# Kernel tuning notes

Measured on AMD Instinct MI355X. Metric: run time of the kernel, lower is better.

## Reference

```python
import jax, jax.numpy as jnp
import numpy as np

C = 512
CQ = C // 8
B, H, W = 8, 64, 64


def conv1x1(x, w, b):
    # x: [B,Cin,H,W], w: [Cout,Cin], b: [Cout]
    return jnp.einsum('bchw,oc->bohw', x, w) + b[None, :, None, None]


def setup_inputs() -> dict:
    key = jax.random.key(0)
    ks = jax.random.split(key, 16)
    s = 0.02
    return {
        'x': jax.random.normal(ks[0], (B, C, H, W), dtype=jnp.float32),
        # position attention params
        'pq_w': jax.random.normal(ks[1], (CQ, C), dtype=jnp.float32) * s,
        'pq_b': jnp.zeros((CQ,), dtype=jnp.float32),
        'pk_w': jax.random.normal(ks[2], (CQ, C), dtype=jnp.float32) * s,
        'pk_b': jnp.zeros((CQ,), dtype=jnp.float32),
        'pv_w': jax.random.normal(ks[3], (C, C), dtype=jnp.float32) * s,
        'pv_b': jnp.zeros((C,), dtype=jnp.float32),
        # channel attention params
        'cq_w': jax.random.normal(ks[4], (CQ, C), dtype=jnp.float32) * s,
        'cq_b': jnp.zeros((CQ,), dtype=jnp.float32),
        'ck_w': jax.random.normal(ks[5], (CQ, C), dtype=jnp.float32) * s,
        'ck_b': jnp.zeros((CQ,), dtype=jnp.float32),
        'cv_w': jax.random.normal(ks[6], (CQ, C), dtype=jnp.float32) * s,
        'cv_b': jnp.zeros((CQ,), dtype=jnp.float32),
        'co_w': jax.random.normal(ks[7], (C, CQ), dtype=jnp.float32) * s,
        'co_b': jnp.zeros((C,), dtype=jnp.float32),
    }


def reference(x, pq_w, pq_b, pk_w, pk_b, pv_w, pv_b,
              cq_w, cq_b, ck_w, ck_b, cv_w, cv_b, co_w, co_b):
    b, c, h, w = x.shape
    hw = h * w

    # ---- Position attention ----
    q = conv1x1(x, pq_w, pq_b).reshape(b, CQ, hw)   # [B,Cq,HW]
    k = conv1x1(x, pk_w, pk_b).reshape(b, CQ, hw)   # [B,Cq,HW]
    v = conv1x1(x, pv_w, pv_b).reshape(b, c, hw)    # [B,C,HW]
    # energy[b,i,j] = sum_c q[b,c,i] * k[b,c,j]; softmax over j
    energy = jnp.einsum('bci,bcj->bij', q, k)       # [B,HW,HW]
    attn = jax.nn.softmax(energy, axis=-1)
    # out[b,c,j] = sum_i v[b,c,i] * attn[b,i,j]  (value @ attention)
    pos_out = jnp.einsum('bci,bij->bcj', v, attn).reshape(b, c, h, w)

    # ---- Channel attention ----
    cq = conv1x1(x, cq_w, cq_b).reshape(b, CQ, hw)  # [B,Cq,HW]
    ck = conv1x1(x, ck_w, ck_b).reshape(b, CQ, hw)  # [B,Cq,HW]
    cv = conv1x1(x, cv_w, cv_b).reshape(b, CQ, hw)  # [B,Cq,HW]
    c_energy = jnp.einsum('bpn,bqn->bpq', cq, ck)   # [B,Cq,Cq]
    c_attn = jax.nn.softmax(c_energy, axis=-1)
    c_out = jnp.einsum('bpq,bqn->bpn', c_attn, cv).reshape(b, CQ, h, w)
    chan_out = conv1x1(c_out, co_w, co_b)           # [B,C,H,W]

    return pos_out + chan_out
```

## Files before the change

### kernel.cpp

```cpp
#include <hip/hip_runtime.h>
#include <stdint.h>


#define LOG2E 1.44269504088896340736f

typedef __attribute__((ext_vector_type(8))) __bf16 bf16x8;
typedef __attribute__((ext_vector_type(4))) float floatx4;
typedef __attribute__((ext_vector_type(2))) float floatx2;
typedef __attribute__((ext_vector_type(2))) unsigned int uint2v;

static __device__ __forceinline__ unsigned short f2bf(float f) {
    union { float f; uint32_t u; } v; v.f = f;
    uint32_t r = v.u + 0x7fffu + ((v.u >> 16) & 1u);
    return (unsigned short)(r >> 16);
}

static __device__ __forceinline__ unsigned int pack_bf16(float a, float b) {
    union { float f; uint32_t u; } x, y; x.f = a; y.f = b;
    return __builtin_amdgcn_perm(y.u + 0x8000u, x.u + 0x8000u, 0x07060302u);
}

template<int BM, int BN, bool OUT_BF16, bool ATOMIC, int SPECIAL = 0>
__global__ __launch_bounds__(256) void tn_gemm(
    const unsigned short* __restrict__ A, int lda, long sA,
    const unsigned short* __restrict__ B, int ldb, long sB,
    void* __restrict__ C, int ldc, long sC,
    const float* __restrict__ bias_m, const float* __restrict__ bias_n,
    const float* __restrict__ scale_n, long sScale,
    int K, int kchunks)
{
    constexpr int PK = 72;
    __shared__ unsigned short As[BM * PK];
    __shared__ unsigned short Bs[BN * PK];
    const int bz = blockIdx.z;
    const int b  = bz / kchunks;
    const int kc = bz % kchunks;
    const int m0 = blockIdx.y * BM;
    const int n0 = blockIdx.x * BN;
    const unsigned short* Ab = A + (long)b * sA + (long)m0 * lda + (long)kc * K;
    const unsigned short* Bb = B + (long)b * sB + (long)n0 * ldb + (long)kc * K;
    const int tid = threadIdx.x;
    const int lane = tid & 63, wave = tid >> 6;
    const int l15 = lane & 15, quad = lane >> 4;
    constexpr int NT  = BN / 16;
    constexpr int MPW = BM / 64;
    constexpr int AL  = BM / 32;
    constexpr int BL  = BN / 32;

    const floatx4 vz = {0.f, 0.f, 0.f, 0.f};
    floatx4 acc[MPW][NT];
    for (int i = 0; i < MPW; ++i) for (int j = 0; j < NT; ++j) acc[i][j] = vz;

    const int nK = K >> 6;
    for (int k0 = 0; k0 < nK; ++k0) {
        floatx4 ar[AL], br[BL];
#pragma unroll
        for (int L = 0; L < AL; ++L) {
            int flat = L * 2048 + tid * 8;
            ar[L] = *(const floatx4*)(Ab + (long)(flat >> 6) * lda + (k0 << 6) + (flat & 63));
        }
#pragma unroll
        for (int L = 0; L < BL; ++L) {
            int flat = L * 2048 + tid * 8;
            br[L] = *(const floatx4*)(Bb + (long)(flat >> 6) * ldb + (k0 << 6) + (flat & 63));
        }
        __syncthreads();
#pragma unroll
        for (int L = 0; L < AL; ++L) {
            int flat = L * 2048 + tid * 8;
            *(floatx4*)&As[(flat >> 6) * PK + (flat & 63)] = ar[L];
        }
#pragma unroll
        for (int L = 0; L < BL; ++L) {
            int flat = L * 2048 + tid * 8;
            *(floatx4*)&Bs[(flat >> 6) * PK + (flat & 63)] = br[L];
        }
        __syncthreads();
#pragma unroll
        for (int ks = 0; ks < 2; ++ks) {
            bf16x8 af[MPW];
#pragma unroll
            for (int mi = 0; mi < MPW; ++mi)
                af[mi] = *(const bf16x8*)&As[((wave * MPW + mi) * 16 + l15) * PK + ks * 32 + quad * 8];
#pragma unroll
            for (int nt = 0; nt < NT; ++nt) {
                bf16x8 bf = *(const bf16x8*)&Bs[(nt * 16 + l15) * PK + ks * 32 + quad * 8];
#pragma unroll
                for (int mi = 0; mi < MPW; ++mi)
                    acc[mi][nt] = __builtin_amdgcn_mfma_f32_16x16x32_bf16(af[mi], bf, acc[mi][nt], 0, 0, 0);
            }
        }
    }
#pragma unroll
    for (int mi = 0; mi < MPW; ++mi) {
        const int mb = m0 + (wave * MPW + mi) * 16 + quad * 4;
#pragma unroll
        for (int nt = 0; nt < NT; ++nt) {
            const int n = n0 + nt * 16 + l15;
            const float bn = bias_n ? bias_n[n] : 0.f;
            const float cs = scale_n ? scale_n[(long)b * sScale + n] : 1.f;
            floatx4 a = acc[mi][nt];
#pragma unroll
            for (int r = 0; r < 4; ++r) {
                const int m = mb + r;
                float v = (a[r] + (bias_m ? bias_m[m] : 0.f) + bn) * cs;
                long idx;
                if (SPECIAL == 1)
                    idx = (long)b * sC + ((long)(n >> 7) * 65536 + (m >> 4) * 2048
                        + ((n >> 5) & 3) * 512 + (m & 15) * 32 + ((n >> 3) & 3) * 8 + (n & 7));
                else if (SPECIAL == 2) {
                    if (n < 64)
                        idx = (long)b * sC + ((long)(m >> 4) * 1024 + (n >> 5) * 512
                            + (m & 15) * 32 + ((n >> 3) & 3) * 8 + (n & 7));
                    else
                        idx = (long)b * sC + (long)(n >> 6) * 262144 + (long)m * 64 + (n & 63);
                } else
                    idx = (long)b * sC + (long)m * ldc + n;
                if (ATOMIC)         atomicAdd((float*)C + idx, v);
                else if (OUT_BF16)  ((unsigned short*)C)[idx] = f2bf(v);
                else                ((float*)C)[idx] = v;
            }
        }
    }
}

__global__ __launch_bounds__(512, 4) void rowsum_kernel(
    const unsigned short* __restrict__ qkvT, float* __restrict__ rcl)
{
    __shared__ unsigned short Ks[2][128 * 72];
    const int b  = blockIdx.x;
    const int i0 = blockIdx.y * 128;
    const unsigned short* qv = qkvT + (long)b * 786432;
    const unsigned short* kb = qkvT + (long)b * 786432 + 262144;
    const int tid = threadIdx.x, lane = tid & 63, wave = tid >> 6;
    const int l15 = lane & 15, quad = lane >> 4;

    bf16x8 af[2];
#pragma unroll
    for (int ks = 0; ks < 2; ++ks)
        af[ks] = *(const bf16x8*)(qv + (long)((i0 >> 4) + wave) * 1024 + ks * 512 + (l15 * 4 + quad) * 8);

#pragma unroll
    for (int p = 0; p < 2; ++p) {
        int flat = p * 4096 + tid * 8;
        *(floatx4*)&Ks[0][(flat >> 6) * 72 + (flat & 63)] = *(const floatx4*)(kb + flat);
    }
    float rs[4] = {0.f, 0.f, 0.f, 0.f};
    const floatx4 vz = {0.f, 0.f, 0.f, 0.f};
    __syncthreads();

    for (int jb = 0; jb < 32; ++jb) {
        const int cur = jb & 1;
        floatx4 stage[2];
        if (jb < 31) {
#pragma unroll
            for (int p = 0; p < 2; ++p) {
                int flat = p * 4096 + tid * 8;
                stage[p] = *(const floatx4*)(kb + (jb + 1) * 8192 + flat);
            }
        }
        floatx4 e[8];
#pragma unroll
        for (int nt = 0; nt < 8; ++nt) e[nt] = vz;
#pragma unroll
        for (int ks = 0; ks < 2; ++ks)
#pragma unroll
            for (int nt = 0; nt < 8; ++nt) {
                bf16x8 bf = *(const bf16x8*)&Ks[cur][(nt * 16 + l15) * 72 + ks * 32 + quad * 8];
                e[nt] = __builtin_amdgcn_mfma_f32_16x16x32_bf16(af[ks], bf, e[nt], 0, 0, 0);
            }
#pragma unroll
        for (int nt = 0; nt < 8; ++nt)
#pragma unroll
            for (int r = 0; r < 4; ++r)
                rs[r] += exp2f(e[nt][r]);
        if (jb < 31) {
#pragma unroll
            for (int p = 0; p < 2; ++p) {
                int flat = p * 4096 + tid * 8;
                *(floatx4*)&Ks[1 - cur][(flat >> 6) * 72 + (flat & 63)] = stage[p];
            }
        }
        __syncthreads();
    }
#pragma unroll
    for (int r = 0; r < 4; ++r) {
        float v = rs[r];
        v += __shfl_xor(v, 1); v += __shfl_xor(v, 2);
        v += __shfl_xor(v, 4); v += __shfl_xor(v, 8);
        if (l15 == 0)
            rcl[(long)b * 4096 + i0 + wave * 16 + quad * 4 + r] = 1.0f / v;
    }
}

__global__ __launch_bounds__(512, 4) void pos_attn_kernel(
    const unsigned short* __restrict__ qkvT, const unsigned short* __restrict__ vP,
    const unsigned short* __restrict__ wco, const unsigned short* __restrict__ coT,
    const float* __restrict__ co_b, float* __restrict__ out)
{
    __shared__ unsigned short Ks[64 * 72];
    __shared__ unsigned short Ps[2][64 * 136];
    const int b  = blockIdx.x;
    const int j0 = blockIdx.y * 64;
    const unsigned short* qb = qkvT + (long)b * 786432;
    const unsigned short* kb = qkvT + (long)b * 786432 + 262144 + (long)j0 * 64;
    const unsigned short* vb = vP + (long)b * 512 * 4096;
    const int tid = threadIdx.x, lane = tid & 63, wave = tid >> 6;
    const int l15 = lane & 15, quad = lane >> 4;
    const int il = wave * 16 + quad * 4;
    const int lfrag = (l15 * 4 + quad) * 8;
    const int vfrag = l15 * 32 + quad * 8;

    {
        int flat = tid * 8;
        *(floatx4*)&Ks[(flat >> 6) * 72 + (flat & 63)] = *(const floatx4*)(kb + flat);
    }
    const floatx4 vz = {0.f, 0.f, 0.f, 0.f};
    floatx4 oacc[4][4];
#pragma unroll
    for (int mi = 0; mi < 4; ++mi) for (int nt = 0; nt < 4; ++nt) oacc[mi][nt] = vz;
    __syncthreads();

    auto e_phase = [&](int ib, int buf) {
        const unsigned short* qr = qb + (long)(ib * 8 + wave) * 1024;
        bf16x8 a0 = *(const bf16x8*)(qr + lfrag);
        bf16x8 a1 = *(const bf16x8*)(qr + 512 + lfrag);
        floatx4 e[4];
#pragma unroll
        for (int nt = 0; nt < 4; ++nt) e[nt] = vz;
#pragma unroll
        for (int nt = 0; nt < 4; ++nt) {
            bf16x8 bf = *(const bf16x8*)&Ks[(nt * 16 + l15) * 72 + quad * 8];
            e[nt] = __builtin_amdgcn_mfma_f32_16x16x32_bf16(a0, bf, e[nt], 0, 0, 0);
        }
#pragma unroll
        for (int nt = 0; nt < 4; ++nt) {
            bf16x8 bf = *(const bf16x8*)&Ks[(nt * 16 + l15) * 72 + 32 + quad * 8];
            e[nt] = __builtin_amdgcn_mfma_f32_16x16x32_bf16(a1, bf, e[nt], 0, 0, 0);
        }
#pragma unroll
        for (int nt = 0; nt < 4; ++nt) {
            uint2v p;
            p.x = pack_bf16(exp2f(e[nt][0]), exp2f(e[nt][1]));
            p.y = pack_bf16(exp2f(e[nt][2]), exp2f(e[nt][3]));
            *(uint2v*)&Ps[buf][(nt * 16 + l15) * 136 + il] = p;
        }
    };

    e_phase(0, 0);
    __syncthreads();

    for (int ib = 0; ib < 32; ++ib) {
        const int cur = ib & 1;
        const unsigned short* vt = vb + (long)ib * 65536 + (wave * 4) * 2048 + vfrag;
#pragma unroll
        for (int ks = 0; ks < 4; ++ks) {
            bf16x8 af[4];
#pragma unroll
            for (int mi = 0; mi < 4; ++mi)
                af[mi] = *(const bf16x8*)(vt + mi * 2048 + ks * 512);
#pragma unroll
            for (int nt = 0; nt < 4; ++nt) {
                bf16x8 bf = *(const bf16x8*)&Ps[cur][(nt * 16 + l15) * 136 + ks * 32 + quad * 8];
#pragma unroll
                for (int mi = 0; mi < 4; ++mi)
                    oacc[mi][nt] = __builtin_amdgcn_mfma_f32_16x16x32_bf16(af[mi], bf, oacc[mi][nt], 0, 0, 0);
            }
        }
        if (ib < 31) e_phase(ib + 1, 1 - cur);
        __syncthreads();
    }

    const unsigned short* cob = coT + ((long)b * 4096 + j0) * 64;
#pragma unroll
    for (int ks = 0; ks < 2; ++ks) {
        bf16x8 aw[4];
#pragma unroll
        for (int mi = 0; mi < 4; ++mi)
            aw[mi] = *(const bf16x8*)(wco + (long)((wave * 4 + mi) * 16 + l15) * 64 + ks * 32 + quad * 8);
#pragma unroll
        for (int nt = 0; nt < 4; ++nt) {
            bf16x8 bf = *(const bf16x8*)(cob + (long)(nt * 16 + l15) * 64 + ks * 32 + quad * 8);
#pragma unroll
            for (int mi = 0; mi < 4; ++mi)
                oacc[mi][nt] = __builtin_amdgcn_mfma_f32_16x16x32_bf16(aw[mi], bf, oacc[mi][nt], 0, 0, 0);
        }
    }
#pragma unroll
    for (int mi = 0; mi < 4; ++mi) {
        const int c = (wave * 4 + mi) * 16 + quad * 4;
#pragma unroll
        for (int nt = 0; nt < 4; ++nt) {
            const int j = j0 + nt * 16 + l15;
#pragma unroll
            for (int r = 0; r < 4; ++r)
                out[((long)b * 512 + c + r) * 4096 + j] = oacc[mi][nt][r] + co_b[c + r];
        }
    }
}

__global__ __launch_bounds__(256) void transpose_x(
    const float* __restrict__ x, unsigned short* __restrict__ xT)
{
    __shared__ unsigned short T[64 * 66];
    const int b  = blockIdx.z;
    const int n0 = blockIdx.x * 64;
    const int c0 = blockIdx.y * 64;
    const int tid = threadIdx.x;
    const int r8 = tid >> 5;
    const int col2 = (tid & 31) * 2;
#pragma unroll
    for (int k = 0; k < 8; ++k) {
        const int c = r8 + k * 8;
        floatx2 v = *(const floatx2*)(x + ((long)(b * 512 + c0 + c)) * 4096 + n0 + col2);
        *(unsigned int*)&T[c * 66 + col2] = pack_bf16(v.x, v.y);
    }
    __syncthreads();
#pragma unroll
    for (int k = 0; k < 8; ++k) {
        const int n = r8 + k * 8;
        unsigned int pk = (unsigned int)T[col2 * 66 + n] | ((unsigned int)T[(col2 + 1) * 66 + n] << 16);
        *(unsigned int*)(xT + ((long)(b * 4096 + n0 + n)) * 512 + c0 + col2) = pk;
    }
}

__global__ __launch_bounds__(256) void convert_weights(
    const float* __restrict__ pq_w, const float* __restrict__ pk_w,
    const float* __restrict__ pv_w, const float* __restrict__ cq_w,
    const float* __restrict__ ck_w, const float* __restrict__ cv_w,
    const float* __restrict__ co_w,
    const float* __restrict__ pq_b, const float* __restrict__ pk_b,
    const float* __restrict__ cv_b, const float* __restrict__ cq_b,
    const float* __restrict__ ck_b,
    unsigned short* __restrict__ dst, float* __restrict__ biases)
{
    const int total = 458752;
    const int gtid = blockIdx.x * 256 + threadIdx.x;
    for (int i = gtid; i < total; i += gridDim.x * 256) {
        float v;
        if (i < 98304) {
            int r = i >> 9, k = i & 511;
            if (r < 64)       v = pq_w[r * 512 + k] * LOG2E;
            else if (r < 128) v = pk_w[(r - 64) * 512 + k];
            else              v = cv_w[(r - 128) * 512 + k];
        } else if (i < 163840) {
            int j = i - 98304; int r = j >> 9, k = j & 511;
            v = (r < 64) ? cq_w[r * 512 + k] : ck_w[(r - 64) * 512 + k];
        } else if (i < 425984) v = pv_w[i - 163840];
        else                   v = co_w[i - 425984];
        dst[i] = f2bf(v);
    }
    if (gtid < 320) {
        float v;
        if (gtid < 64)       v = pq_b[gtid] * LOG2E;
        else if (gtid < 128) v = pk_b[gtid - 64];
        else if (gtid < 192) v = cv_b[gtid - 128];
        else if (gtid < 256) v = cq_b[gtid - 192];
        else                 v = ck_b[gtid - 256];
        biases[gtid] = v;
    }
}

__global__ __launch_bounds__(64) void chan_softmax(
    const float* __restrict__ ce, unsigned short* __restrict__ ca)
{
    const int p = blockIdx.x, b = blockIdx.y, q = threadIdx.x;
    const long base = ((long)b * 64 + p) * 64;
    float v = ce[base + q];
    float m = v;
#pragma unroll
    for (int s = 32; s >= 1; s >>= 1) m = fmaxf(m, __shfl_xor(m, s));
    float e = exp2f((v - m) * LOG2E);
    float sum = e;
#pragma unroll
    for (int s = 32; s >= 1; s >>= 1) sum += __shfl_xor(sum, s);
    ca[base + q] = f2bf(e / sum);
}

extern "C" void kernel_launch(void* const* d_in, const int* in_sizes, int n_in,
                              void* d_out, int out_size, void* d_ws, size_t ws_size,
                              hipStream_t stream) {
    const float* x    = (const float*)d_in[0];
    const float* pv_b = (const float*)d_in[6];
    const float* co_b = (const float*)d_in[14];
    float* out = (float*)d_out;
    char* ws = (char*)d_ws;

    constexpr long OFF_XT   = 0;
    constexpr long OFF_QKV  = 33554432;
    constexpr long OFF_VP   = OFF_QKV + 12582912;
    constexpr long OFF_CQCK = OFF_VP + 33554432;
    constexpr long OFF_COT  = OFF_CQCK + 8388608;
    constexpr long OFF_RCL  = OFF_COT + 4194304;
    constexpr long OFF_CE   = OFF_RCL + 131072;
    constexpr long OFF_CAT  = OFF_CE + 131072;
    constexpr long OFF_WB   = OFF_CAT + 65536;
    constexpr long OFF_BIAS = OFF_WB + 917504;

    unsigned short* xT   = (unsigned short*)(ws + OFF_XT);
    unsigned short* qkvT = (unsigned short*)(ws + OFF_QKV);
    unsigned short* vP   = (unsigned short*)(ws + OFF_VP);
    unsigned short* cqck = (unsigned short*)(ws + OFF_CQCK);
    unsigned short* coT  = (unsigned short*)(ws + OFF_COT);
    float*          rcl  = (float*)(ws + OFF_RCL);
    float*          ce   = (float*)(ws + OFF_CE);
    unsigned short* cat  = (unsigned short*)(ws + OFF_CAT);
    unsigned short* wb   = (unsigned short*)(ws + OFF_WB);
    float*          bias = (float*)(ws + OFF_BIAS);
    unsigned short* wqkv  = wb;
    unsigned short* wcqck = wb + 98304;
    unsigned short* wv    = wb + 163840;
    unsigned short* wco   = wb + 425984;
    float* bqkv  = bias;
    float* bcqck = bias + 192;

    convert_weights<<<dim3(64), 256, 0, stream>>>(
        (const float*)d_in[1], (const float*)d_in[3], (const float*)d_in[5],
        (const float*)d_in[7], (const float*)d_in[9], (const float*)d_in[11],
        (const float*)d_in[13],
        (const float*)d_in[2], (const float*)d_in[4], (const float*)d_in[12],
        (const float*)d_in[8], (const float*)d_in[10], wb, bias);
    transpose_x<<<dim3(64, 8, 8), 256, 0, stream>>>(x, xT);

    tn_gemm<128, 192, true, false, 2><<<dim3(1, 32, 8), 256, 0, stream>>>(
        xT, 512, 2097152L, wqkv, 512, 0L, qkvT, 192, 786432L,
        nullptr, bqkv, nullptr, 0L, 512, 1);
    tn_gemm<128, 128, true, false><<<dim3(32, 1, 8), 256, 0, stream>>>(
        wcqck, 512, 0L, xT, 512, 2097152L, cqck, 4096, 524288L,
        bcqck, nullptr, nullptr, 0L, 512, 1);

    rowsum_kernel<<<dim3(8, 32), 512, 0, stream>>>(qkvT, rcl);

    tn_gemm<128, 128, true, false, 1><<<dim3(32, 4, 8), 256, 0, stream>>>(
        wv, 512, 0L, xT, 512, 2097152L, vP, 4096, 2097152L,
        pv_b, nullptr, rcl, 4096L, 512, 1);

    hipMemsetAsync(ce, 0, 8 * 64 * 64 * sizeof(float), stream);
    tn_gemm<64, 64, false, true><<<dim3(1, 1, 64), 256, 0, stream>>>(
        cqck, 4096, 524288L, cqck + 262144, 4096, 524288L, ce, 64, 4096L,
        nullptr, nullptr, nullptr, 0L, 512, 8);
    chan_softmax<<<dim3(64, 8), 64, 0, stream>>>(ce, cat);
    tn_gemm<128, 64, true, false><<<dim3(1, 32, 8), 256, 0, stream>>>(
        qkvT + 524288, 64, 786432L, cat, 64, 4096L, coT, 64, 262144L,
        nullptr, nullptr, nullptr, 0L, 64, 1);

    pos_attn_kernel<<<dim3(8, 64), 512, 0, stream>>>(qkvT, vP, wco, coT, co_b, out);
}
```

Baseline: 487.0 us.

## Fuse QKV and channel q/k projections into one GEMM, store K in fragment layout

The q/k/v and channel q/k 1x1-conv GEMMs are merged into a single 64x64-tiled GEMM whose epilogue routes columns to qkvT or to the cqck buffer. K is also stored in MFMA fragment-packed order. With that layout the rowsum kernel drops its LDS double-buffering and reads K fragments straight from global memory using small 128-thread blocks, and the pos_attn K load is remapped to match. Smaller tiles raise the block count, and one launch is removed. The cost is scattered transposed stores for the cqck output and more redundant global K reads in rowsum.

```diff
diff --git a/kernel.cpp b/kernel.cpp
--- a/kernel.cpp
+++ b/kernel.cpp
@@ -25,6 +25,7 @@
     const unsigned short* __restrict__ A, int lda, long sA,
     const unsigned short* __restrict__ B, int ldb, long sB,
     void* __restrict__ C, int ldc, long sC,
+    void* __restrict__ C2, long sC2,
     const float* __restrict__ bias_m, const float* __restrict__ bias_n,
     const float* __restrict__ scale_n, long sScale,
     int K, int kchunks)
@@ -104,93 +105,84 @@
             for (int r = 0; r < 4; ++r) {
                 const int m = mb + r;
                 float v = (a[r] + (bias_m ? bias_m[m] : 0.f) + bn) * cs;
-                long idx;
-                if (SPECIAL == 1)
-                    idx = (long)b * sC + ((long)(n >> 7) * 65536 + (m >> 4) * 2048
-                        + ((n >> 5) & 3) * 512 + (m & 15) * 32 + ((n >> 3) & 3) * 8 + (n & 7));
-                else if (SPECIAL == 2) {
-                    if (n < 64)
-                        idx = (long)b * sC + ((long)(m >> 4) * 1024 + (n >> 5) * 512
-                            + (m & 15) * 32 + ((n >> 3) & 3) * 8 + (n & 7));
+                if (SPECIAL == 2) {
+                    unsigned short* dp;
+                    long idx2;
+                    if (n < 64) {
+                        dp = (unsigned short*)C;
+                        idx2 = (long)b * sC + ((long)(m >> 4) * 1024 + (n >> 5) * 512
+                             + (m & 15) * 32 + ((n >> 3) & 3) * 8 + (n & 7));
+                    } else if (n < 128) {
+                        const int kk = n - 64;
+                        dp = (unsigned short*)C;
+                        idx2 = (long)b * sC + 262144 + ((long)(m >> 4) * 1024 + (kk >> 5) * 512
+                             + (m & 15) * 32 + ((kk >> 3) & 3) * 8 + (kk & 7));
+                    } else if (n < 192) {
+                        dp = (unsigned short*)C;
+                        idx2 = (long)b * sC + 524288 + (long)m * 64 + (n - 128);
+                    } else {
+                        dp = (unsigned short*)C2;
+                        idx2 = (long)b * sC2 + (long)(n - 192) * 4096 + m;
+                    }
+                    dp[idx2] = f2bf(v);
+                } else {
+                    long idx;
+                    if (SPECIAL == 1)
+                        idx = (long)b * sC + ((long)(n >> 7) * 65536 + (m >> 4) * 2048
+                            + ((n >> 5) & 3) * 512 + (m & 15) * 32 + ((n >> 3) & 3) * 8 + (n & 7));
                     else
-                        idx = (long)b * sC + (long)(n >> 6) * 262144 + (long)m * 64 + (n & 63);
-                } else
-                    idx = (long)b * sC + (long)m * ldc + n;
-                if (ATOMIC)         atomicAdd((float*)C + idx, v);
-                else if (OUT_BF16)  ((unsigned short*)C)[idx] = f2bf(v);
-                else                ((float*)C)[idx] = v;
+                        idx = (long)b * sC + (long)m * ldc + n;
+                    if (ATOMIC)         atomicAdd((float*)C + idx, v);
+                    else if (OUT_BF16)  ((unsigned short*)C)[idx] = f2bf(v);
+                    else                ((float*)C)[idx] = v;
+                }
             }
         }
     }
 }
 
-__global__ __launch_bounds__(512, 4) void rowsum_kernel(
+__global__ __launch_bounds__(128, 4) void rowsum_kernel(
     const unsigned short* __restrict__ qkvT, float* __restrict__ rcl)
 {
-    __shared__ unsigned short Ks[2][128 * 72];
     const int b  = blockIdx.x;
-    const int i0 = blockIdx.y * 128;
+    const int i0 = blockIdx.y * 64;
     const unsigned short* qv = qkvT + (long)b * 786432;
-    const unsigned short* kb = qkvT + (long)b * 786432 + 262144;
+    const unsigned short* kf = qkvT + (long)b * 786432 + 262144;
     const int tid = threadIdx.x, lane = tid & 63, wave = tid >> 6;
     const int l15 = lane & 15, quad = lane >> 4;
-
-    bf16x8 af[2];
-#pragma unroll
-    for (int ks = 0; ks < 2; ++ks)
-        af[ks] = *(const bf16x8*)(qv + (long)((i0 >> 4) + wave) * 1024 + ks * 512 + (l15 * 4 + quad) * 8);
-
-#pragma unroll
-    for (int p = 0; p < 2; ++p) {
-        int flat = p * 4096 + tid * 8;
-        *(floatx4*)&Ks[0][(flat >> 6) * 72 + (flat & 63)] = *(const floatx4*)(kb + flat);
-    }
-    float rs[4] = {0.f, 0.f, 0.f, 0.f};
+    const int lfrag = l15 * 32 + quad * 8;
+
+    bf16x8 af[2][2];
+#pragma unroll
+    for (int t = 0; t < 2; ++t)
+#pragma unroll
+        for (int ks = 0; ks < 2; ++ks)
+            af[t][ks] = *(const bf16x8*)(qv + (long)((i0 >> 4) + wave * 2 + t) * 1024
+                                             + ks * 512 + lfrag);
+
+    float rs[2][4] = {{0.f,0.f,0.f,0.f},{0.f,0.f,0.f,0.f}};
     const floatx4 vz = {0.f, 0.f, 0.f, 0.f};
-    __syncthreads();
-
-    for (int jb = 0; jb < 32; ++jb) {
-        const int cur = jb & 1;
-        floatx4 stage[2];
-        if (jb < 31) {
-#pragma unroll
-            for (int p = 0; p < 2; ++p) {
-                int flat = p * 4096 + tid * 8;
-                stage[p] = *(const floatx4*)(kb + (jb + 1) * 8192 + flat);
-            }
-        }
-        floatx4 e[8];
-#pragma unroll
-        for (int nt = 0; nt < 8; ++nt) e[nt] = vz;
-#pragma unroll
-        for (int ks = 0; ks < 2; ++ks)
-#pragma unroll
-            for (int nt = 0; nt < 8; ++nt) {
-                bf16x8 bf = *(const bf16x8*)&Ks[cur][(nt * 16 + l15) * 72 + ks * 32 + quad * 8];
-                e[nt] = __builtin_amdgcn_mfma_f32_16x16x32_bf16(af[ks], bf, e[nt], 0, 0, 0);
-            }
-#pragma unroll
-        for (int nt = 0; nt < 8; ++nt)
-#pragma unroll
-            for (int r = 0; r < 4; ++r)
-                rs[r] += exp2f(e[nt][r]);
-        if (jb < 31) {
-#pragma unroll
-            for (int p = 0; p < 2; ++p) {
-                int flat = p * 4096 + tid * 8;
-                *(floatx4*)&Ks[1 - cur][(flat >> 6) * 72 + (flat & 63)] = stage[p];
-            }
-        }
-        __syncthreads();
-    }
-#pragma unroll
-    for (int r = 0; r < 4; ++r) {
-        float v = rs[r];
-        v += __shfl_xor(v, 1); v += __shfl_xor(v, 2);
-        v += __shfl_xor(v, 4); v += __shfl_xor(v, 8);
-        if (l15 == 0)
-            rcl[(long)b * 4096 + i0 + wave * 16 + quad * 4 + r] = 1.0f / v;
-    }
+    for (int jt = 0; jt < 256; ++jt) {
+        bf16x8 b0 = *(const bf16x8*)(kf + jt * 1024 + lfrag);
+        bf16x8 b1 = *(const bf16x8*)(kf + jt * 1024 + 512 + lfrag);
+#pragma unroll
+        for (int t = 0; t < 2; ++t) {
+            floatx4 e = __builtin_amdgcn_mfma_f32_16x16x32_bf16(af[t][0], b0, vz, 0, 0, 0);
+            e = __builtin_amdgcn_mfma_f32_16x16x32_bf16(af[t][1], b1, e, 0, 0, 0);
+#pragma unroll
+            for (int r = 0; r < 4; ++r) rs[t][r] += exp2f(e[r]);
+        }
+    }
+#pragma unroll
+    for (int t = 0; t < 2; ++t)
+#pragma unroll
+        for (int r = 0; r < 4; ++r) {
+            float v = rs[t][r];
+            v += __shfl_xor(v, 1); v += __shfl_xor(v, 2);
+            v += __shfl_xor(v, 4); v += __shfl_xor(v, 8);
+            if (l15 == 0)
+                rcl[(long)b * 4096 + i0 + (wave * 2 + t) * 16 + quad * 4 + r] = 1.0f / v;
+        }
 }
 
 __global__ __launch_bounds__(512, 4) void pos_attn_kernel(
@@ -203,7 +195,7 @@
     const int b  = blockIdx.x;
     const int j0 = blockIdx.y * 64;
     const unsigned short* qb = qkvT + (long)b * 786432;
-    const unsigned short* kb = qkvT + (long)b * 786432 + 262144 + (long)j0 * 64;
+    const unsigned short* kf = qkvT + (long)b * 786432 + 262144 + (long)(j0 >> 4) * 1024;
     const unsigned short* vb = vP + (long)b * 512 * 4096;
     const int tid = threadIdx.x, lane = tid & 63, wave = tid >> 6;
     const int l15 = lane & 15, quad = lane >> 4;
@@ -212,8 +204,10 @@
     const int vfrag = l15 * 32 + quad * 8;
 
     {
-        int flat = tid * 8;
-        *(floatx4*)&Ks[(flat >> 6) * 72 + (flat & 63)] = *(const floatx4*)(kb + flat);
+        int g = tid * 8;
+        int row = ((g >> 10) << 4) | ((g >> 5) & 15);
+        int col = ((g >> 9) & 1) * 32 + ((g >> 3) & 3) * 8;
+        *(floatx4*)&Ks[row * 72 + col] = *(const floatx4*)(kf + g);
     }
     const floatx4 vz = {0.f, 0.f, 0.f, 0.f};
     floatx4 oacc[4][4];
@@ -407,12 +401,8 @@
     unsigned short* cat  = (unsigned short*)(ws + OFF_CAT);
     unsigned short* wb   = (unsigned short*)(ws + OFF_WB);
     float*          bias = (float*)(ws + OFF_BIAS);
-    unsigned short* wqkv  = wb;
-    unsigned short* wcqck = wb + 98304;
     unsigned short* wv    = wb + 163840;
     unsigned short* wco   = wb + 425984;
-    float* bqkv  = bias;
-    float* bcqck = bias + 192;
 
     convert_weights<<<dim3(64), 256, 0, stream>>>(
         (const float*)d_in[1], (const float*)d_in[3], (const float*)d_in[5],
@@ -422,27 +412,24 @@
         (const float*)d_in[8], (const float*)d_in[10], wb, bias);
     transpose_x<<<dim3(64, 8, 8), 256, 0, stream>>>(x, xT);
 
-    tn_gemm<128, 192, true, false, 2><<<dim3(1, 32, 8), 256, 0, stream>>>(
-        xT, 512, 2097152L, wqkv, 512, 0L, qkvT, 192, 786432L,
-        nullptr, bqkv, nullptr, 0L, 512, 1);
-    tn_gemm<128, 128, true, false><<<dim3(32, 1, 8), 256, 0, stream>>>(
-        wcqck, 512, 0L, xT, 512, 2097152L, cqck, 4096, 524288L,
-        bcqck, nullptr, nullptr, 0L, 512, 1);
-
-    rowsum_kernel<<<dim3(8, 32), 512, 0, stream>>>(qkvT, rcl);
+    tn_gemm<64, 64, true, false, 2><<<dim3(5, 64, 8), 256, 0, stream>>>(
+        xT, 512, 2097152L, wb, 512, 0L, qkvT, 192, 786432L,
+        cqck, 524288L, nullptr, bias, nullptr, 0L, 512, 1);
+
+    rowsum_kernel<<<dim3(8, 64), 128, 0, stream>>>(qkvT, rcl);
 
     tn_gemm<128, 128, true, false, 1><<<dim3(32, 4, 8), 256, 0, stream>>>(
         wv, 512, 0L, xT, 512, 2097152L, vP, 4096, 2097152L,
-        pv_b, nullptr, rcl, 4096L, 512, 1);
+        nullptr, 0L, pv_b, nullptr, rcl, 4096L, 512, 1);
 
     hipMemsetAsync(ce, 0, 8 * 64 * 64 * sizeof(float), stream);
     tn_gemm<64, 64, false, true><<<dim3(1, 1, 64), 256, 0, stream>>>(
         cqck, 4096, 524288L, cqck + 262144, 4096, 524288L, ce, 64, 4096L,
-        nullptr, nullptr, nullptr, 0L, 512, 8);
+        nullptr, 0L, nullptr, nullptr, nullptr, 0L, 512, 8);
     chan_softmax<<<dim3(64, 8), 64, 0, stream>>>(ce, cat);
-    tn_gemm<128, 64, true, false><<<dim3(1, 32, 8), 256, 0, stream>>>(
+    tn_gemm<64, 64, true, false><<<dim3(1, 64, 8), 256, 0, stream>>>(
         qkvT + 524288, 64, 786432L, cat, 64, 4096L, coT, 64, 262144L,
-        nullptr, nullptr, nullptr, 0L, 64, 1);
+        nullptr, 0L, nullptr, nullptr, nullptr, 0L, 64, 1);
 
     pos_attn_kernel<<<dim3(8, 64), 512, 0, stream>>>(qkvT, vP, wco, coT, co_b, out);
 }
```

New measurement: 504.5 us. +3.6%, slower.
